# Optimization experiments

Hardware: AMD Instinct MI355X
Metric: run time of the kernel (lower is better)

## Reference

```python
import jax, jax.numpy as jnp
import numpy as np

DIM, HEADS, MLP_RATIO = 384, 6, 4.0
HEAD_DIM = DIM // HEADS
HID = int(DIM * MLP_RATIO)
EPS = 1e-5


def _layer_norm(x, g, b):
    m = jnp.mean(x, axis=-1, keepdims=True)
    v = jnp.mean(jnp.square(x - m), axis=-1, keepdims=True)
    return (x - m) * jax.lax.rsqrt(v + EPS) * g + b


def setup_inputs() -> dict:
    key = jax.random.key(0)
    ks = jax.random.split(key, 16)
    B, N, C = 4, 2048, DIM
    s = 0.02
    return {
        "x": jax.random.normal(ks[0], (B, N, C), dtype=jnp.float32),
        "ln1_g": jnp.ones((C,), jnp.float32),
        "ln1_b": jnp.zeros((C,), jnp.float32),
        "qkv_w": jax.random.normal(ks[1], (C, 3 * C), jnp.float32) * s,  # [in, out]
        "qkv_b": jnp.zeros((3 * C,), jnp.float32),
        "proj_w": jax.random.normal(ks[2], (C, C), jnp.float32) * s,
        "proj_b": jnp.zeros((C,), jnp.float32),
        "ln2_g": jnp.ones((C,), jnp.float32),
        "ln2_b": jnp.zeros((C,), jnp.float32),
        "fc1_w": jax.random.normal(ks[3], (C, HID), jnp.float32) * s,
        "fc1_b": jnp.zeros((HID,), jnp.float32),
        "fc2_w": jax.random.normal(ks[4], (HID, C), jnp.float32) * s,
        "fc2_b": jnp.zeros((C,), jnp.float32),
    }


def reference(x, ln1_g, ln1_b, qkv_w, qkv_b, proj_w, proj_b,
              ln2_g, ln2_b, fc1_w, fc1_b, fc2_w, fc2_b):
    B, N, C = x.shape
    scale = HEAD_DIM ** (-0.5)

    # --- attention branch (pre-norm) ---
    h = _layer_norm(x, ln1_g, ln1_b)
    qkv = (h @ qkv_w + qkv_b).reshape(B, N, 3, HEADS, HEAD_DIM)
    qkv = jnp.transpose(qkv, (2, 0, 3, 1, 4))  # [3, B, H, N, D]
    q, k, v = qkv[0], qkv[1], qkv[2]
    attn = jnp.einsum("bhnd,bhmd->bhnm", q, k) * scale
    attn = jax.nn.softmax(attn, axis=-1)
    out = jnp.einsum("bhnm,bhmd->bhnd", attn, v)
    out = jnp.transpose(out, (0, 2, 1, 3)).reshape(B, N, C)
    x = x + (out @ proj_w + proj_b)

    # --- MLP branch (pre-norm) ---
    h = _layer_norm(x, ln2_g, ln2_b)
    h = jax.nn.gelu(h @ fc1_w + fc1_b, approximate=False)
    x = x + (h @ fc2_w + fc2_b)
    return x
```

## Files before the change

kernel.cpp:

```cpp
#include <hip/hip_runtime.h>

typedef unsigned short u16;
typedef unsigned int u32;
typedef __bf16 bf16x8_t __attribute__((ext_vector_type(8)));
typedef float f32x4 __attribute__((ext_vector_type(4)));
typedef float f32x16 __attribute__((ext_vector_type(16)));

__device__ __forceinline__ u16 f2b(float f) {
  union { float f; u32 u; } v; v.f = f;
  u32 r = v.u + 0x7fffu + ((v.u >> 16) & 1u);
  return (u16)(r >> 16);
}

__device__ __forceinline__ u32 pkbf(float a, float b) {
  union { __bf16 h[2]; u32 u; } v;
  v.h[0] = (__bf16)a; v.h[1] = (__bf16)b;
  return v.u;
}

__device__ __forceinline__ f32x4 mfma16(uint4 a, uint4 b, f32x4 c) {
  return __builtin_amdgcn_mfma_f32_16x16x32_bf16(
      __builtin_bit_cast(bf16x8_t, a), __builtin_bit_cast(bf16x8_t, b), c, 0, 0, 0);
}

__device__ __forceinline__ f32x16 mfma32(uint4 a, uint4 b, f32x16 c) {
  return __builtin_amdgcn_mfma_f32_32x32x16_bf16(
      __builtin_bit_cast(bf16x8_t, a), __builtin_bit_cast(bf16x8_t, b), c, 0, 0, 0);
}

__device__ __forceinline__ void plswap(u32& a, u32& b) {
  asm("v_permlane32_swap_b32 %0, %1" : "+v"(a), "+v"(b));
}

__device__ __forceinline__ void load_lds16(const void* g, void* l) {
  __builtin_amdgcn_global_load_lds(
      (const __attribute__((address_space(1))) unsigned int*)g,
      (__attribute__((address_space(3))) unsigned int*)l, 16, 0, 0);
}

__global__ __launch_bounds__(256) void convT4_k(
    const float* __restrict__ w0, u16* __restrict__ t0_,
    const float* __restrict__ w1, u16* __restrict__ t1_,
    const float* __restrict__ w2, u16* __restrict__ t2_,
    const float* __restrict__ w3, u16* __restrict__ t3_) {
  __shared__ u16 L[64][68];
  int tile = blockIdx.x, tid = threadIdx.x;
  const float* w; u16* wt; int K, N, rel;
  if (tile < 108)      { w = w0; wt = t0_; K = 384;  N = 1152; rel = tile; }
  else if (tile < 144) { w = w1; wt = t1_; K = 384;  N = 384;  rel = tile - 108; }
  else if (tile < 288) { w = w2; wt = t2_; K = 384;  N = 1536; rel = tile - 144; }
  else                 { w = w3; wt = t3_; K = 1536; N = 384;  rel = tile - 288; }
  int ntx = N >> 6;
  int tk = (rel / ntx) << 6, tn = (rel - (rel / ntx) * ntx) << 6;

  int r = tid >> 2, c0 = (tid & 3) << 4;
  const float* src = w + (size_t)(tk + r) * N + tn + c0;
#pragma unroll
  for (int j = 0; j < 16; j += 4) {
    float4 a = *(const float4*)(src + j);
    L[r][c0 + j + 0] = f2b(a.x);
    L[r][c0 + j + 1] = f2b(a.y);
    L[r][c0 + j + 2] = f2b(a.z);
    L[r][c0 + j + 3] = f2b(a.w);
  }
  __syncthreads();
  int n = tid >> 2, k0 = (tid & 3) << 4;
  u16 tmp[16];
#pragma unroll
  for (int j = 0; j < 16; j++) tmp[j] = L[k0 + j][n];
  u16* dst = wt + (size_t)(tn + n) * K + tk + k0;
  *(uint4*)dst = *(const uint4*)(tmp);
  *(uint4*)(dst + 8) = *(const uint4*)(tmp + 8);
}

__global__ __launch_bounds__(256) void ln_k(const float* __restrict__ x,
                                            const float* __restrict__ g,
                                            const float* __restrict__ bta,
                                            u16* __restrict__ out) {
  int lane = threadIdx.x & 63, wid = threadIdx.x >> 6;
  int row = blockIdx.x * 4 + wid;
  const float* xr = x + (size_t)row * 384;
  float v[6];
  float s = 0.f;
#pragma unroll
  for (int i = 0; i < 6; i++) { v[i] = xr[i * 64 + lane]; s += v[i]; }
#pragma unroll
  for (int off = 32; off >= 1; off >>= 1) s += __shfl_xor(s, off);
  float mean = s * (1.0f / 384.0f);
  float vs = 0.f;
#pragma unroll
  for (int i = 0; i < 6; i++) { float d = v[i] - mean; vs += d * d; }
#pragma unroll
  for (int off = 32; off >= 1; off >>= 1) vs += __shfl_xor(vs, off);
  float rstd = rsqrtf(vs * (1.0f / 384.0f) + 1e-5f);
  u16* orow = out + (size_t)row * 384;
#pragma unroll
  for (int i = 0; i < 6; i++) {
    int c = i * 64 + lane;
    orow[c] = f2b((v[i] - mean) * rstd * g[c] + bta[c]);
  }
}

template <int EPI, int MR>
__global__ __launch_bounds__(256) void gemm_k(
    const u16* __restrict__ A, const u16* __restrict__ Bt,
    const float* __restrict__ bias, const float* __restrict__ res,
    void* __restrict__ outp, int M, int Nn, int K,
    u16* __restrict__ qp, u16* __restrict__ kp, u16* __restrict__ vtp) {
  constexpr int BMt = MR * 32;
  constexpr int AWV = BMt / 32;
  __shared__ __align__(16) u16 As[2][BMt * 64];
  __shared__ __align__(16) u16 Bs[2][64 * 64];
  int tid = threadIdx.x;
  int lane = tid & 63, wid = tid >> 6;
  int li = lane & 15, lg = lane >> 4;
  int wr = wid >> 1, wc = wid & 1;
  int row0 = blockIdx.y * BMt, col0 = blockIdx.x * 64;

  int lr = lane >> 3;
  int sc8 = ((lane & 7) ^ lr) * 8;

  f32x4 z = {0.f, 0.f, 0.f, 0.f};
  f32x4 acc[MR][2];
#pragma unroll
  for (int m = 0; m < MR; m++)
#pragma unroll
    for (int n = 0; n < 2; n++) acc[m][n] = z;

  auto STAGE = [&](int buf, int k0) {
#pragma unroll
    for (int j = 0; j < AWV; j++) {
      int ia = wid * AWV + j;
      load_lds16(A + (size_t)(row0 + ia * 8 + lr) * K + k0 + sc8,
                 (char*)As[buf] + ia * 1024);
    }
#pragma unroll
    for (int j = 0; j < 2; j++) {
      int ib = wid * 2 + j;
      load_lds16(Bt + (size_t)(col0 + ib * 8 + lr) * K + k0 + sc8,
                 (char*)Bs[buf] + ib * 1024);
    }
  };

  int nsteps = K >> 6;
  STAGE(0, 0);

  int buf = 0;
  for (int t = 0; t < nsteps; t++) {
    if (t + 1 < nsteps) {
      STAGE(buf ^ 1, (t + 1) * 64);
      if constexpr (MR == 4)
        asm volatile("s_waitcnt vmcnt(6)" ::: "memory");
      else
        asm volatile("s_waitcnt vmcnt(4)" ::: "memory");
    } else {
      asm volatile("s_waitcnt vmcnt(0)" ::: "memory");
    }
    __builtin_amdgcn_s_barrier();
    asm volatile("" ::: "memory");
    const char* Asb = (const char*)As[buf];
    const char* Bsb = (const char*)Bs[buf];
#pragma unroll
    for (int kk = 0; kk < 2; kk++) {
      uint4 af[MR], bf[2];
#pragma unroll
      for (int m = 0; m < MR; m++) {
        int r = wr * (MR * 16) + m * 16 + li;
        af[m] = *(const uint4*)(Asb + r * 128 +
                                ((kk * 64 + lg * 16) ^ ((r & 7) << 4)));
      }
#pragma unroll
      for (int n = 0; n < 2; n++) {
        int c = wc * 32 + n * 16 + li;
        bf[n] = *(const uint4*)(Bsb + c * 128 +
                                ((kk * 64 + lg * 16) ^ ((c & 7) << 4)));
      }
#pragma unroll
      for (int m = 0; m < MR; m++)
#pragma unroll
        for (int n = 0; n < 2; n++)
          acc[m][n] = mfma16(af[m], bf[n], acc[m][n]);
    }
    asm volatile("" ::: "memory");
    __builtin_amdgcn_s_barrier();
    buf ^= 1;
  }

#pragma unroll
  for (int m = 0; m < MR; m++) {
#pragma unroll
    for (int n = 0; n < 2; n++) {
#pragma unroll
      for (int j = 0; j < 4; j++) {
        int r = row0 + wr * (MR * 16) + m * 16 + lg * 4 + j;
        int c = col0 + wc * 32 + n * 16 + li;
        float v = acc[m][n][j] + bias[c];
        if (EPI == 0) {
          ((float*)outp)[(size_t)r * Nn + c] = v + res[(size_t)r * Nn + c];
        } else if (EPI == 1) {
          float e = __expf(-1.5957691f * v * (1.f + 0.044715f * v * v));
          ((u16*)outp)[(size_t)r * Nn + c] = f2b(v / (1.f + e));
        } else {
          int t = c / 384;
          int c2 = c - t * 384;
          int hh = c2 >> 6, d = c2 & 63;
          int bb = r >> 11, nn = r & 2047;
          size_t bh = (size_t)bb * 6 + hh;
          int tile = nn >> 5;
          if (t == 2) {
            int kvl = nn & 31;
            int kvHalf = (kvl >> 4) & 1, h2 = (kvl >> 3) & 1, jj = kvl & 7;
            int dTile = d >> 5, l31 = d & 31;
            vtp[(((bh * 64 + tile) * 2 + dTile) * 2 + kvHalf) * 512 +
                (l31 + h2 * 32) * 8 + jj] = f2b(v);
          } else {
            int chunk = d >> 4, h2 = (d >> 3) & 1, e = d & 7;
            int l31 = nn & 31;
            size_t off = ((bh * 64 + tile) * 4 + chunk) * 512 +
                         (l31 + h2 * 32) * 8 + e;
            if (t == 0) qp[off] = f2b(v * 0.125f);
            else        kp[off] = f2b(v);
          }
        }
      }
    }
  }
}

__global__ __launch_bounds__(256, 3) void attn_k(const u16* __restrict__ q,
                                                 const u16* __restrict__ k,
                                                 const u16* __restrict__ vt,
                                                 u16* __restrict__ out) {
  __shared__ __align__(16) float Ol[3][2][16][64];
  __shared__ float Ls[3][64];

  int tid = threadIdx.x;
  int lane = tid & 63, wid = tid >> 6;
  int l31 = lane & 31, hi = lane >> 5;
  int bid = blockIdx.x;
  int nid = (bid & 7) * 192 + (bid >> 3);
  int bh = nid >> 6, qTile = nid & 63;
  int b = bh / 6, hh = bh - b * 6;
  int qb = qTile * 32;

  const u16* qp_ = q + (size_t)(bh * 64 + qTile) * 2048 + lane * 8;
  const u16* kp_ = k + (size_t)(bh * 64 + wid * 16) * 2048 + lane * 8;
  const u16* vp_ = vt + (size_t)(bh * 64 + wid * 16) * 2048 + lane * 8;

  uint4 qf[4], kf[4];
#pragma unroll
  for (int c = 0; c < 4; c++) qf[c] = *(const uint4*)(qp_ + c * 512);
#pragma unroll
  for (int c = 0; c < 4; c++) kf[c] = *(const uint4*)(kp_ + c * 512);
  kp_ += 2048;

  f32x16 o0, o1;
#pragma unroll
  for (int r = 0; r < 16; r++) { o0[r] = 0.f; o1[r] = 0.f; }
  float lsum = 0.f;

#pragma unroll
  for (int t = 0; t < 16; t++) {
    uint4 vf0 = *(const uint4*)(vp_);
    uint4 vf1 = *(const uint4*)(vp_ + 512);
    uint4 vf2 = *(const uint4*)(vp_ + 1024);
    uint4 vf3 = *(const uint4*)(vp_ + 1536);
    uint4 kn[4];
    if (t < 15) {
#pragma unroll
      for (int c = 0; c < 4; c++) kn[c] = *(const uint4*)(kp_ + c * 512);
    }

    f32x16 s;
#pragma unroll
    for (int r = 0; r < 16; r++) s[r] = 0.f;
    s = mfma32(kf[0], qf[0], s);
    s = mfma32(kf[1], qf[1], s);
    s = mfma32(kf[2], qf[2], s);
    s = mfma32(kf[3], qf[3], s);

    float p[16];
#pragma unroll
    for (int r = 0; r < 16; r++) p[r] = __expf(s[r]);

    float a0 = (p[0] + p[1]) + (p[2] + p[3]);
    float a1 = (p[4] + p[5]) + (p[6] + p[7]);
    float a2 = (p[8] + p[9]) + (p[10] + p[11]);
    float a3 = (p[12] + p[13]) + (p[14] + p[15]);
    lsum += (a0 + a1) + (a2 + a3);

    u32 u[8];
#pragma unroll
    for (int i = 0; i < 8; i++) u[i] = pkbf(p[2 * i], p[2 * i + 1]);
    plswap(u[0], u[2]); plswap(u[1], u[3]);
    plswap(u[4], u[6]); plswap(u[5], u[7]);
    uint4 pa0 = {u[0], u[1], u[2], u[3]};
    uint4 pa1 = {u[4], u[5], u[6], u[7]};

    o0 = mfma32(pa0, vf0, o0);
    o0 = mfma32(pa1, vf1, o0);
    o1 = mfma32(pa0, vf2, o1);
    o1 = mfma32(pa1, vf3, o1);

    if (t < 15) {
#pragma unroll
      for (int c = 0; c < 4; c++) kf[c] = kn[c];
    }
    kp_ += 2048;
    vp_ += 2048;
  }

  lsum += __shfl_xor(lsum, 32);

  if (wid) {
#pragma unroll
    for (int r = 0; r < 16; r++) {
      Ol[wid - 1][0][r][lane] = o0[r];
      Ol[wid - 1][1][r][lane] = o1[r];
    }
    Ls[wid - 1][lane] = lsum;
  }
  __syncthreads();
  if (wid == 0) {
#pragma unroll
    for (int w = 0; w < 3; w++) lsum += Ls[w][lane];
#pragma unroll
    for (int r = 0; r < 16; r++)
#pragma unroll
      for (int w = 0; w < 3; w++) {
        o0[r] += Ol[w][0][r][lane];
        o1[r] += Ol[w][1][r][lane];
      }
    float rl = 1.0f / lsum;
#pragma unroll
    for (int r = 0; r < 16; r++) {
      int qo = (r & 3) + 8 * (r >> 2) + hi * 4;
      float rlq = __shfl(rl, qo, 64);
      int row = b * 2048 + qb + qo;
      out[(size_t)row * 384 + hh * 64 + l31] = f2b(o0[r] * rlq);
      out[(size_t)row * 384 + hh * 64 + 32 + l31] = f2b(o1[r] * rlq);
    }
  }
}

extern "C" void kernel_launch(void* const* d_in, const int* in_sizes, int n_in,
                              void* d_out, int out_size, void* d_ws,
                              size_t ws_size, hipStream_t stream) {
  const float* x      = (const float*)d_in[0];
  const float* ln1_g  = (const float*)d_in[1];
  const float* ln1_b  = (const float*)d_in[2];
  const float* qkv_w  = (const float*)d_in[3];
  const float* qkv_b  = (const float*)d_in[4];
  const float* proj_w = (const float*)d_in[5];
  const float* proj_b = (const float*)d_in[6];
  const float* ln2_g  = (const float*)d_in[7];
  const float* ln2_b  = (const float*)d_in[8];
  const float* fc1_w  = (const float*)d_in[9];
  const float* fc1_b  = (const float*)d_in[10];
  const float* fc2_w  = (const float*)d_in[11];
  const float* fc2_b  = (const float*)d_in[12];
  float* out = (float*)d_out;

  char* p = (char*)d_ws;
  u16* qkvwt  = (u16*)p;  p += (size_t)1152 * 384 * 2;
  u16* projwt = (u16*)p;  p += (size_t)384 * 384 * 2;
  u16* fc1wt  = (u16*)p;  p += (size_t)1536 * 384 * 2;
  u16* fc2wt  = (u16*)p;  p += (size_t)384 * 1536 * 2;
  float* x1   = (float*)p; p += (size_t)8192 * 384 * 4;
  u16* reg1   = (u16*)p;  p += (size_t)8192 * 384 * 2;
  u16* reg2   = (u16*)p;  p += (size_t)8192 * 1536 * 2;
  u16* qd  = reg2;
  u16* kd  = reg2 + (size_t)24 * 2048 * 64;
  u16* vtd = kd + (size_t)24 * 2048 * 64;
  u16* h3  = reg2;

  convT4_k<<<432, 256, 0, stream>>>(qkv_w, qkvwt, proj_w, projwt,
                                    fc1_w, fc1wt, fc2_w, fc2wt);

  ln_k<<<2048, 256, 0, stream>>>(x, ln1_g, ln1_b, reg1);
  gemm_k<2, 4><<<dim3(18, 64), 256, 0, stream>>>(
      reg1, qkvwt, qkv_b, nullptr, nullptr, 8192, 1152, 384, qd, kd, vtd);
  attn_k<<<dim3(1536), 256, 0, stream>>>(qd, kd, vtd, reg1);
  gemm_k<0, 2><<<dim3(6, 128), 256, 0, stream>>>(
      reg1, projwt, proj_b, x, x1, 8192, 384, 384, nullptr, nullptr, nullptr);
  ln_k<<<2048, 256, 0, stream>>>(x1, ln2_g, ln2_b, reg1);
  gemm_k<1, 4><<<dim3(24, 64), 256, 0, stream>>>(
      reg1, fc1wt, fc1_b, nullptr, h3, 8192, 1536, 384, nullptr, nullptr, nullptr);
  gemm_k<0, 2><<<dim3(6, 128), 256, 0, stream>>>(
      h3, fc2wt, fc2_b, x1, out, 8192, 384, 1536, nullptr, nullptr, nullptr);
}
```

Baseline: 140.1 us.

## Triple-buffer GEMM with BK=32, widen N tiles, prefetch V and use exp2 softmax

The GEMM kernel moves from a double-buffered 64-wide K step to a three-stage ring of 32-wide K slices. This removes the trailing barrier per iteration, and the swizzle pattern changes to match. A new NR template parameter doubles the N tile for the QKV and FC1 GEMMs, which halves their grid, and launch bounds now request 3 waves per SIMD. In attention, V fragments are prefetched one step ahead like K, and exp is replaced with exp2 by folding log2(e) into the Q scale. The trade-off is higher register pressure and fewer blocks for the large GEMMs.

```diff
diff --git a/kernel.cpp b/kernel.cpp
--- a/kernel.cpp
+++ b/kernel.cpp
@@ -36,6 +36,15 @@
   __builtin_amdgcn_global_load_lds(
       (const __attribute__((address_space(1))) unsigned int*)g,
       (__attribute__((address_space(3))) unsigned int*)l, 16, 0, 0);
+}
+
+template <int N>
+__device__ __forceinline__ void waitvm() {
+  if constexpr (N == 0) asm volatile("s_waitcnt vmcnt(0)" ::: "memory");
+  else if constexpr (N == 2) asm volatile("s_waitcnt vmcnt(2)" ::: "memory");
+  else if constexpr (N == 4) asm volatile("s_waitcnt vmcnt(4)" ::: "memory");
+  else if constexpr (N == 6) asm volatile("s_waitcnt vmcnt(6)" ::: "memory");
+  else asm volatile("s_waitcnt vmcnt(8)" ::: "memory");
 }
 
 __global__ __launch_bounds__(256) void convT4_k(
@@ -101,99 +110,97 @@
   }
 }
 
-template <int EPI, int MR>
-__global__ __launch_bounds__(256) void gemm_k(
+template <int EPI, int MR, int NR>
+__global__ __launch_bounds__(256, 3) void gemm_k(
     const u16* __restrict__ A, const u16* __restrict__ Bt,
     const float* __restrict__ bias, const float* __restrict__ res,
     void* __restrict__ outp, int M, int Nn, int K,
     u16* __restrict__ qp, u16* __restrict__ kp, u16* __restrict__ vtp) {
   constexpr int BMt = MR * 32;
-  constexpr int AWV = BMt / 32;
-  __shared__ __align__(16) u16 As[2][BMt * 64];
-  __shared__ __align__(16) u16 Bs[2][64 * 64];
+  constexpr int BNt = NR * 32;
+  constexpr int AW = MR / 2;
+  constexpr int BW = NR / 2;
+  __shared__ __align__(16) u16 As[3][BMt * 32];
+  __shared__ __align__(16) u16 Bs[3][BNt * 32];
   int tid = threadIdx.x;
   int lane = tid & 63, wid = tid >> 6;
   int li = lane & 15, lg = lane >> 4;
   int wr = wid >> 1, wc = wid & 1;
-  int row0 = blockIdx.y * BMt, col0 = blockIdx.x * 64;
-
-  int lr = lane >> 3;
-  int sc8 = ((lane & 7) ^ lr) * 8;
+  int row0 = blockIdx.y * BMt, col0 = blockIdx.x * BNt;
+
+  int lr4 = lane >> 2;
+  int sc4 = (((lane & 3) ^ (lr4 & 3) ^ ((lane >> 4) & 1))) * 8;
 
   f32x4 z = {0.f, 0.f, 0.f, 0.f};
-  f32x4 acc[MR][2];
+  f32x4 acc[MR][NR];
 #pragma unroll
   for (int m = 0; m < MR; m++)
 #pragma unroll
-    for (int n = 0; n < 2; n++) acc[m][n] = z;
+    for (int n = 0; n < NR; n++) acc[m][n] = z;
 
   auto STAGE = [&](int buf, int k0) {
 #pragma unroll
-    for (int j = 0; j < AWV; j++) {
-      int ia = wid * AWV + j;
-      load_lds16(A + (size_t)(row0 + ia * 8 + lr) * K + k0 + sc8,
+    for (int j = 0; j < AW; j++) {
+      int ia = wid * AW + j;
+      load_lds16(A + (size_t)(row0 + ia * 16 + lr4) * K + k0 + sc4,
                  (char*)As[buf] + ia * 1024);
     }
 #pragma unroll
-    for (int j = 0; j < 2; j++) {
-      int ib = wid * 2 + j;
-      load_lds16(Bt + (size_t)(col0 + ib * 8 + lr) * K + k0 + sc8,
+    for (int j = 0; j < BW; j++) {
+      int ib = wid * BW + j;
+      load_lds16(Bt + (size_t)(col0 + ib * 16 + lr4) * K + k0 + sc4,
                  (char*)Bs[buf] + ib * 1024);
     }
   };
 
-  int nsteps = K >> 6;
+  int nsteps = K >> 5;
   STAGE(0, 0);
-
-  int buf = 0;
+  STAGE(1, 32);
+
+  int cur = 0;
   for (int t = 0; t < nsteps; t++) {
-    if (t + 1 < nsteps) {
-      STAGE(buf ^ 1, (t + 1) * 64);
-      if constexpr (MR == 4)
-        asm volatile("s_waitcnt vmcnt(6)" ::: "memory");
-      else
-        asm volatile("s_waitcnt vmcnt(4)" ::: "memory");
-    } else {
-      asm volatile("s_waitcnt vmcnt(0)" ::: "memory");
-    }
+    if (t + 1 < nsteps) waitvm<AW + BW>();
+    else waitvm<0>();
     __builtin_amdgcn_s_barrier();
     asm volatile("" ::: "memory");
-    const char* Asb = (const char*)As[buf];
-    const char* Bsb = (const char*)Bs[buf];
-#pragma unroll
-    for (int kk = 0; kk < 2; kk++) {
-      uint4 af[MR], bf[2];
-#pragma unroll
-      for (int m = 0; m < MR; m++) {
-        int r = wr * (MR * 16) + m * 16 + li;
-        af[m] = *(const uint4*)(Asb + r * 128 +
-                                ((kk * 64 + lg * 16) ^ ((r & 7) << 4)));
-      }
-#pragma unroll
-      for (int n = 0; n < 2; n++) {
-        int c = wc * 32 + n * 16 + li;
-        bf[n] = *(const uint4*)(Bsb + c * 128 +
-                                ((kk * 64 + lg * 16) ^ ((c & 7) << 4)));
-      }
-#pragma unroll
-      for (int m = 0; m < MR; m++)
-#pragma unroll
-        for (int n = 0; n < 2; n++)
-          acc[m][n] = mfma16(af[m], bf[n], acc[m][n]);
-    }
+    if (t + 2 < nsteps) {
+      int nx = cur + 2; if (nx >= 3) nx -= 3;
+      STAGE(nx, (t + 2) * 32);
+    }
+    const char* Asb = (const char*)As[cur];
+    const char* Bsb = (const char*)Bs[cur];
+    uint4 af[MR], bf[NR];
+#pragma unroll
+    for (int m = 0; m < MR; m++) {
+      int r = wr * (MR * 16) + m * 16 + li;
+      af[m] = *(const uint4*)(
+          Asb + r * 64 +
+          ((lg * 16) ^ ((r & 3) << 4) ^ (((r >> 2) & 1) << 4)));
+    }
+#pragma unroll
+    for (int n = 0; n < NR; n++) {
+      int c = wc * (NR * 16) + n * 16 + li;
+      bf[n] = *(const uint4*)(
+          Bsb + c * 64 +
+          ((lg * 16) ^ ((c & 3) << 4) ^ (((c >> 2) & 1) << 4)));
+    }
+#pragma unroll
+    for (int m = 0; m < MR; m++)
+#pragma unroll
+      for (int n = 0; n < NR; n++)
+        acc[m][n] = mfma16(af[m], bf[n], acc[m][n]);
     asm volatile("" ::: "memory");
-    __builtin_amdgcn_s_barrier();
-    buf ^= 1;
+    cur = (cur == 2) ? 0 : cur + 1;
   }
 
 #pragma unroll
   for (int m = 0; m < MR; m++) {
 #pragma unroll
-    for (int n = 0; n < 2; n++) {
+    for (int n = 0; n < NR; n++) {
 #pragma unroll
       for (int j = 0; j < 4; j++) {
         int r = row0 + wr * (MR * 16) + m * 16 + lg * 4 + j;
-        int c = col0 + wc * 32 + n * 16 + li;
+        int c = col0 + wc * (NR * 16) + n * 16 + li;
         float v = acc[m][n][j] + bias[c];
         if (EPI == 0) {
           ((float*)outp)[(size_t)r * Nn + c] = v + res[(size_t)r * Nn + c];
@@ -218,7 +225,7 @@
             int l31 = nn & 31;
             size_t off = ((bh * 64 + tile) * 4 + chunk) * 512 +
                          (l31 + h2 * 32) * 8 + e;
-            if (t == 0) qp[off] = f2b(v * 0.125f);
+            if (t == 0) qp[off] = f2b(v * 0.18033688f);
             else        kp[off] = f2b(v);
           }
         }
@@ -239,20 +246,23 @@
   int l31 = lane & 31, hi = lane >> 5;
   int bid = blockIdx.x;
   int nid = (bid & 7) * 192 + (bid >> 3);
-  int bh = nid >> 6, qTile = nid & 63;
+  int bh = nid >> 6, qT = nid & 63;
   int b = bh / 6, hh = bh - b * 6;
-  int qb = qTile * 32;
-
-  const u16* qp_ = q + (size_t)(bh * 64 + qTile) * 2048 + lane * 8;
-  const u16* kp_ = k + (size_t)(bh * 64 + wid * 16) * 2048 + lane * 8;
-  const u16* vp_ = vt + (size_t)(bh * 64 + wid * 16) * 2048 + lane * 8;
-
-  uint4 qf[4], kf[4];
+  int qb = qT * 32;
+
+  const u16* qp_ = q + ((size_t)bh * 64 + qT) * 2048 + lane * 8;
+  const u16* kp_ = k + ((size_t)bh * 64 + wid * 16) * 2048 + lane * 8;
+  const u16* vp_ = vt + ((size_t)bh * 64 + wid * 16) * 2048 + lane * 8;
+
+  uint4 qf[4], kf[4], vf[4];
 #pragma unroll
   for (int c = 0; c < 4; c++) qf[c] = *(const uint4*)(qp_ + c * 512);
 #pragma unroll
   for (int c = 0; c < 4; c++) kf[c] = *(const uint4*)(kp_ + c * 512);
+#pragma unroll
+  for (int c = 0; c < 4; c++) vf[c] = *(const uint4*)(vp_ + c * 512);
   kp_ += 2048;
+  vp_ += 2048;
 
   f32x16 o0, o1;
 #pragma unroll
@@ -261,33 +271,26 @@
 
 #pragma unroll
   for (int t = 0; t < 16; t++) {
-    uint4 vf0 = *(const uint4*)(vp_);
-    uint4 vf1 = *(const uint4*)(vp_ + 512);
-    uint4 vf2 = *(const uint4*)(vp_ + 1024);
-    uint4 vf3 = *(const uint4*)(vp_ + 1536);
-    uint4 kn[4];
+    uint4 kn[4], vn[4];
     if (t < 15) {
 #pragma unroll
       for (int c = 0; c < 4; c++) kn[c] = *(const uint4*)(kp_ + c * 512);
+#pragma unroll
+      for (int c = 0; c < 4; c++) vn[c] = *(const uint4*)(vp_ + c * 512);
     }
 
     f32x16 s;
 #pragma unroll
     for (int r = 0; r < 16; r++) s[r] = 0.f;
-    s = mfma32(kf[0], qf[0], s);
-    s = mfma32(kf[1], qf[1], s);
-    s = mfma32(kf[2], qf[2], s);
-    s = mfma32(kf[3], qf[3], s);
+#pragma unroll
+    for (int c = 0; c < 4; c++) s = mfma32(kf[c], qf[c], s);
 
     float p[16];
 #pragma unroll
-    for (int r = 0; r < 16; r++) p[r] = __expf(s[r]);
-
-    float a0 = (p[0] + p[1]) + (p[2] + p[3]);
-    float a1 = (p[4] + p[5]) + (p[6] + p[7]);
-    float a2 = (p[8] + p[9]) + (p[10] + p[11]);
-    float a3 = (p[12] + p[13]) + (p[14] + p[15]);
-    lsum += (a0 + a1) + (a2 + a3);
+    for (int r = 0; r < 16; r++) p[r] = __builtin_amdgcn_exp2f(s[r]);
+    lsum += ((p[0] + p[1]) + (p[2] + p[3])) + ((p[4] + p[5]) + (p[6] + p[7])) +
+            ((p[8] + p[9]) + (p[10] + p[11])) +
+            ((p[12] + p[13]) + (p[14] + p[15]));
 
     u32 u[8];
 #pragma unroll
@@ -297,14 +300,14 @@
     uint4 pa0 = {u[0], u[1], u[2], u[3]};
     uint4 pa1 = {u[4], u[5], u[6], u[7]};
 
-    o0 = mfma32(pa0, vf0, o0);
-    o0 = mfma32(pa1, vf1, o0);
-    o1 = mfma32(pa0, vf2, o1);
-    o1 = mfma32(pa1, vf3, o1);
+    o0 = mfma32(pa0, vf[0], o0);
+    o0 = mfma32(pa1, vf[1], o0);
+    o1 = mfma32(pa0, vf[2], o1);
+    o1 = mfma32(pa1, vf[3], o1);
 
     if (t < 15) {
 #pragma unroll
-      for (int c = 0; c < 4; c++) kf[c] = kn[c];
+      for (int c = 0; c < 4; c++) { kf[c] = kn[c]; vf[c] = vn[c]; }
     }
     kp_ += 2048;
     vp_ += 2048;
@@ -378,14 +381,14 @@
                                     fc1_w, fc1wt, fc2_w, fc2wt);
 
   ln_k<<<2048, 256, 0, stream>>>(x, ln1_g, ln1_b, reg1);
-  gemm_k<2, 4><<<dim3(18, 64), 256, 0, stream>>>(
+  gemm_k<2, 4, 4><<<dim3(9, 64), 256, 0, stream>>>(
       reg1, qkvwt, qkv_b, nullptr, nullptr, 8192, 1152, 384, qd, kd, vtd);
   attn_k<<<dim3(1536), 256, 0, stream>>>(qd, kd, vtd, reg1);
-  gemm_k<0, 2><<<dim3(6, 128), 256, 0, stream>>>(
+  gemm_k<0, 2, 2><<<dim3(6, 128), 256, 0, stream>>>(
       reg1, projwt, proj_b, x, x1, 8192, 384, 384, nullptr, nullptr, nullptr);
   ln_k<<<2048, 256, 0, stream>>>(x1, ln2_g, ln2_b, reg1);
-  gemm_k<1, 4><<<dim3(24, 64), 256, 0, stream>>>(
+  gemm_k<1, 4, 4><<<dim3(12, 64), 256, 0, stream>>>(
       reg1, fc1wt, fc1_b, nullptr, h3, 8192, 1536, 384, nullptr, nullptr, nullptr);
-  gemm_k<0, 2><<<dim3(6, 128), 256, 0, stream>>>(
+  gemm_k<0, 2, 2><<<dim3(6, 128), 256, 0, stream>>>(
       h3, fc2wt, fc2_b, x1, out, 8192, 384, 1536, nullptr, nullptr, nullptr);
 }
```

Measured after the change: 147.8 us. 5.5% more time.
